# Optimization experiments

Measured on AMD Instinct MI355X. Metric: run time of the kernel, lower is better.

The kernel has to match this reference:

```python
import jax, jax.numpy as jnp
import numpy as np

B, No, Nr, D = 128, 128, 512, 512

def setup_inputs() -> dict:
    key = jax.random.key(0)
    ks = jax.random.split(key, 9)
    s = 1.0 / np.sqrt(2 * D)
    s3 = 1.0 / np.sqrt(3 * D)
    return {
        "obj_vecs": jax.random.normal(ks[0], (B, No, D), jnp.float32),
        "attr_vecs": jax.random.normal(ks[1], (B, No, 2 * D), jnp.float32),
        "rela_vecs": jax.random.normal(ks[2], (B, Nr, D), jnp.float32),
        "edges": jax.random.randint(ks[3], (B, Nr, 2), 0, No, jnp.int64),
        "rela_masks": jnp.ones((B, Nr, 1), jnp.float32),
        "W_att": jax.random.uniform(ks[4], (2 * D, D), jnp.float32, -s, s),
        "b_att": jnp.zeros((D,), jnp.float32),
        "W_attr": jax.random.uniform(ks[5], (2 * D, D), jnp.float32, -s, s),
        "b_attr": jnp.zeros((D,), jnp.float32),
        "W_rela": jax.random.uniform(ks[6], (3 * D, D), jnp.float32, -s3, s3),
        "b_rela": jnp.zeros((D,), jnp.float32),
    }

def reference(obj_vecs, attr_vecs, rela_vecs, edges, rela_masks,
              W_att, b_att, W_attr, b_attr, W_rela, b_rela):
    b, no, d = obj_vecs.shape
    # attr projection: (B,No,2d) -> (B,No,d)
    attr = attr_vecs @ W_att + b_att
    # flatten to 2d with per-batch edge offsets
    obj2 = obj_vecs.reshape(-1, d)
    attr2 = attr.reshape(-1, d)
    rela2 = rela_vecs.reshape(-1, d)
    off = (jnp.arange(b, dtype=edges.dtype) * no)[:, None, None]
    e = (edges + off).reshape(-1, 2)
    # attr branch: cat(obj, attr) -> Linear -> ReLU (+ dropout is identity at eval) + residual
    new_attr = jax.nn.relu(jnp.concatenate([obj2, attr2], -1) @ W_attr + b_attr) + attr2
    # rela branch (rela_gnn_type == 0): cat(s, rela, o)
    s_vecs = obj2[e[:, 0]]
    o_vecs = obj2[e[:, 1]]
    t = jnp.concatenate([s_vecs, rela2, o_vecs], -1)
    new_rela = jax.nn.relu(t @ W_rela + b_rela) + rela2
    new_obj = obj_vecs  # passed through unchanged
    return (new_obj,
            new_attr.reshape(b, no, d),
            new_rela.reshape(b, -1, d) * rela_masks)
```

## Files before the change

### kernel.cpp

```cpp
#include <hip/hip_runtime.h>
#include <hip/hip_bf16.h>
#include <stdint.h>

#define C_B   128
#define C_NO  128
#define C_NR  512
#define C_D   512

typedef __attribute__((ext_vector_type(8))) short  short8;
typedef __attribute__((ext_vector_type(4))) float  floatx4;

__device__ __forceinline__ void load_lds16(const void* g, void* lds) {
  __builtin_amdgcn_global_load_lds(
      (const __attribute__((address_space(1))) void*)g,
      (__attribute__((address_space(3))) void*)lds, 16, 0, 0);
}

__device__ __forceinline__ short bfs(float x) {
  __hip_bfloat16 h = __float2bfloat16(x);
  return *reinterpret_cast<short*>(&h);
}

__global__ void transpose_cvt_k(const float* __restrict__ W,
                                __hip_bfloat16* __restrict__ WT, int K, int N) {
  __shared__ float tile[32][33];
  const int k0 = blockIdx.x * 32;
  const int n0 = blockIdx.y * 32;
  const int tx = threadIdx.x & 31;
  const int ty = threadIdx.x >> 5;
#pragma unroll
  for (int i = ty; i < 32; i += 8)
    tile[i][tx] = W[(size_t)(k0 + i) * N + n0 + tx];
  __syncthreads();
#pragma unroll
  for (int i = ty; i < 32; i += 8)
    WT[(size_t)(n0 + i) * K + k0 + tx] = __float2bfloat16(tile[tx][i]);
}

__global__ void copy16_k(const uint4* __restrict__ src, uint4* __restrict__ dst) {
  const size_t i = (size_t)blockIdx.x * blockDim.x + threadIdx.x;
  dst[i] = src[i];
}

template <int MODE, int K>
__global__ __launch_bounds__(256) void gemm_k(
    const float* __restrict__ A0,
    const float* __restrict__ A1,
    const int* __restrict__ edges,
    const __hip_bfloat16* __restrict__ WT,
    const float* __restrict__ bias,
    const float* __restrict__ resid,
    const float* __restrict__ mask,
    float* __restrict__ Cout) {
  constexpr int BK = 32;
  __shared__ __align__(16) __hip_bfloat16 As[128 * BK];
  __shared__ __align__(16) __hip_bfloat16 Bs[128 * BK];
  __shared__ int sRow[128];
  __shared__ int oRow[128];

  const int t = threadIdx.x;
  const int lane = t & 63;
  const int w = t >> 6;
  const int m0 = blockIdx.y * 128;
  const int n0 = blockIdx.x * 128;

  if constexpr (MODE == 2) {
    if (t < 128) {
      const int r = m0 + t;
      const int b = r >> 9;
      sRow[t] = b * C_NO + edges[2 * r];
      oRow[t] = b * C_NO + edges[2 * r + 1];
    }
    __syncthreads();
  }

  const int aRow = t >> 2;
  const int aCol = (t & 3) * 8;

  floatx4 acc[4][4];
#pragma unroll
  for (int i = 0; i < 4; ++i)
#pragma unroll
    for (int j = 0; j < 4; ++j) acc[i][j] = (floatx4)0.0f;

  const int wm = (w >> 1) * 64;
  const int wn = (w & 1) * 64;
  const int fm = lane & 15;
  const int kq = (lane >> 4) * 8;

  for (int kt = 0; kt < K; kt += BK) {
#pragma unroll
    for (int j = 0; j < 2; ++j)
      load_lds16(WT + (size_t)(n0 + j * 64 + aRow) * K + kt + aCol,
                 &Bs[j * 2048 + w * 512]);
#pragma unroll
    for (int j = 0; j < 2; ++j) {
      const int m = j * 64 + aRow;
      const int kg = kt + aCol;
      const float* srcA;
      if constexpr (MODE == 0) {
        srcA = A0 + (size_t)(m0 + m) * K + kg;
      } else if constexpr (MODE == 1) {
        srcA = (kg < C_D) ? A0 + (size_t)(m0 + m) * C_D + kg
                          : A1 + (size_t)(m0 + m) * C_D + (kg - C_D);
      } else {
        const int region = kg >> 9;
        if (region == 0)
          srcA = A0 + (size_t)sRow[m] * C_D + kg;
        else if (region == 1)
          srcA = A1 + (size_t)(m0 + m) * C_D + (kg - C_D);
        else
          srcA = A0 + (size_t)oRow[m] * C_D + (kg - 2 * C_D);
      }
      const float4 f0 = *reinterpret_cast<const float4*>(srcA);
      const float4 f1 = *reinterpret_cast<const float4*>(srcA + 4);
      short8 v;
      v[0] = bfs(f0.x); v[1] = bfs(f0.y); v[2] = bfs(f0.z); v[3] = bfs(f0.w);
      v[4] = bfs(f1.x); v[5] = bfs(f1.y); v[6] = bfs(f1.z); v[7] = bfs(f1.w);
      *reinterpret_cast<short8*>(&As[j * 2048 + t * 8]) = v;
    }
    __syncthreads();

    short8 af[4], bf[4];
#pragma unroll
    for (int mi = 0; mi < 4; ++mi)
      af[mi] = *reinterpret_cast<const short8*>(&As[(wm + mi * 16 + fm) * BK + kq]);
#pragma unroll
    for (int ni = 0; ni < 4; ++ni)
      bf[ni] = *reinterpret_cast<const short8*>(&Bs[(wn + ni * 16 + fm) * BK + kq]);
#pragma unroll
    for (int mi = 0; mi < 4; ++mi)
#pragma unroll
      for (int ni = 0; ni < 4; ++ni)
        acc[mi][ni] =
            __builtin_amdgcn_mfma_f32_16x16x32_bf16(af[mi], bf[ni], acc[mi][ni], 0, 0, 0);
    __syncthreads();
  }

  float bv[4];
#pragma unroll
  for (int ni = 0; ni < 4; ++ni)
    bv[ni] = bias[n0 + wn + ni * 16 + fm];

#pragma unroll
  for (int mi = 0; mi < 4; ++mi) {
    const int rb = m0 + wm + mi * 16 + (lane >> 4) * 4;
#pragma unroll
    for (int i = 0; i < 4; ++i) {
      const int cm = rb + i;
      float mv = 1.0f;
      if constexpr (MODE == 2) mv = mask[cm];
#pragma unroll
      for (int ni = 0; ni < 4; ++ni) {
        const int cn = n0 + wn + ni * 16 + fm;
        float v = acc[mi][ni][i] + bv[ni];
        if constexpr (MODE == 0) {
          Cout[(size_t)cm * C_D + cn] = v;
        } else {
          v = fmaxf(v, 0.0f) + resid[(size_t)cm * C_D + cn];
          if constexpr (MODE == 2) v *= mv;
          Cout[(size_t)cm * C_D + cn] = v;
        }
      }
    }
  }
}

extern "C" void kernel_launch(void* const* d_in, const int* in_sizes, int n_in,
                              void* d_out, int out_size, void* d_ws, size_t ws_size,
                              hipStream_t stream) {
  const float* obj       = (const float*)d_in[0];
  const float* attr_vecs = (const float*)d_in[1];
  const float* rela      = (const float*)d_in[2];
  const int*   edges     = (const int*)d_in[3];
  const float* masks     = (const float*)d_in[4];
  const float* W_att     = (const float*)d_in[5];
  const float* b_att     = (const float*)d_in[6];
  const float* W_attr    = (const float*)d_in[7];
  const float* b_attr    = (const float*)d_in[8];
  const float* W_rela    = (const float*)d_in[9];
  const float* b_rela    = (const float*)d_in[10];

  float* out      = (float*)d_out;
  float* out_obj  = out;
  float* out_attr = out + 8388608;
  float* out_rela = out + 16777216;

  float*          attrS   = out_rela;
  __hip_bfloat16* WT_att  = (__hip_bfloat16*)(out_rela + 8388608);
  __hip_bfloat16* WT_attr = (__hip_bfloat16*)(out_rela + 8650752);
  __hip_bfloat16* WT_rela = (__hip_bfloat16*)out_obj;

  transpose_cvt_k<<<dim3(32, 16), 256, 0, stream>>>(W_att, WT_att, 1024, 512);
  transpose_cvt_k<<<dim3(32, 16), 256, 0, stream>>>(W_attr, WT_attr, 1024, 512);
  transpose_cvt_k<<<dim3(48, 16), 256, 0, stream>>>(W_rela, WT_rela, 1536, 512);

  gemm_k<0, 1024><<<dim3(4, 128), 256, 0, stream>>>(
      attr_vecs, nullptr, nullptr, WT_att, b_att, nullptr, nullptr, attrS);

  gemm_k<1, 1024><<<dim3(4, 128), 256, 0, stream>>>(
      obj, attrS, nullptr, WT_attr, b_attr, attrS, nullptr, out_attr);

  gemm_k<2, 1536><<<dim3(4, 512), 256, 0, stream>>>(
      obj, rela, edges, WT_rela, b_rela, rela, masks, out_rela);

  copy16_k<<<8192, 256, 0, stream>>>((const uint4*)obj, (uint4*)out_obj);
}
```

Baseline: 698.7 us.

## Pre-convert GEMM activations to bf16 and load A tiles via direct LDS loads

Adds a bulk fp32-to-bf16 conversion kernel for obj and attr_vecs, and has the attention GEMM also write a bf16 copy of its output. The three GEMMs then fetch most A-tile data as bf16 through global_load_lds, instead of loading fp32 and converting per tile in registers. Only the rela segment still converts in-kernel. This halves A-operand bytes for the heavily re-read gathered object rows and cuts per-tile conversion ALU work, at the cost of two extra conversion passes and a restructured scratch layout inside the output buffer. Edge-row indices now live in registers instead of shared memory, which removes one barrier.

```diff
diff --git a/kernel.cpp b/kernel.cpp
--- a/kernel.cpp
+++ b/kernel.cpp
@@ -37,6 +37,17 @@
     WT[(size_t)(n0 + i) * K + k0 + tx] = __float2bfloat16(tile[tx][i]);
 }
 
+__global__ void cvt_bf16_k(const float* __restrict__ src,
+                           __hip_bfloat16* __restrict__ dst) {
+  const size_t i = (size_t)blockIdx.x * blockDim.x + threadIdx.x;
+  const float4 f0 = reinterpret_cast<const float4*>(src)[2 * i];
+  const float4 f1 = reinterpret_cast<const float4*>(src)[2 * i + 1];
+  short8 v;
+  v[0] = bfs(f0.x); v[1] = bfs(f0.y); v[2] = bfs(f0.z); v[3] = bfs(f0.w);
+  v[4] = bfs(f1.x); v[5] = bfs(f1.y); v[6] = bfs(f1.z); v[7] = bfs(f1.w);
+  reinterpret_cast<short8*>(dst)[i] = v;
+}
+
 __global__ void copy16_k(const uint4* __restrict__ src, uint4* __restrict__ dst) {
   const size_t i = (size_t)blockIdx.x * blockDim.x + threadIdx.x;
   dst[i] = src[i];
@@ -44,19 +55,19 @@
 
 template <int MODE, int K>
 __global__ __launch_bounds__(256) void gemm_k(
-    const float* __restrict__ A0,
-    const float* __restrict__ A1,
+    const __hip_bfloat16* __restrict__ A0,
+    const __hip_bfloat16* __restrict__ A1,
+    const float* __restrict__ Af32,
     const int* __restrict__ edges,
     const __hip_bfloat16* __restrict__ WT,
     const float* __restrict__ bias,
     const float* __restrict__ resid,
     const float* __restrict__ mask,
-    float* __restrict__ Cout) {
+    float* __restrict__ Cout,
+    __hip_bfloat16* __restrict__ CoutBf) {
   constexpr int BK = 32;
   __shared__ __align__(16) __hip_bfloat16 As[128 * BK];
   __shared__ __align__(16) __hip_bfloat16 Bs[128 * BK];
-  __shared__ int sRow[128];
-  __shared__ int oRow[128];
 
   const int t = threadIdx.x;
   const int lane = t & 63;
@@ -64,18 +75,18 @@
   const int m0 = blockIdx.y * 128;
   const int n0 = blockIdx.x * 128;
 
-  if constexpr (MODE == 2) {
-    if (t < 128) {
-      const int r = m0 + t;
-      const int b = r >> 9;
-      sRow[t] = b * C_NO + edges[2 * r];
-      oRow[t] = b * C_NO + edges[2 * r + 1];
-    }
-    __syncthreads();
-  }
-
   const int aRow = t >> 2;
   const int aCol = (t & 3) * 8;
+
+  int sr0 = 0, sr1 = 0, or0 = 0, or1 = 0;
+  if constexpr (MODE == 2) {
+    const int r0 = m0 + aRow;
+    const int r1 = r0 + 64;
+    sr0 = (r0 >> 9) * C_NO + edges[2 * r0];
+    or0 = (r0 >> 9) * C_NO + edges[2 * r0 + 1];
+    sr1 = (r1 >> 9) * C_NO + edges[2 * r1];
+    or1 = (r1 >> 9) * C_NO + edges[2 * r1 + 1];
+  }
 
   floatx4 acc[4][4];
 #pragma unroll
@@ -95,29 +106,31 @@
                  &Bs[j * 2048 + w * 512]);
 #pragma unroll
     for (int j = 0; j < 2; ++j) {
-      const int m = j * 64 + aRow;
       const int kg = kt + aCol;
-      const float* srcA;
       if constexpr (MODE == 0) {
-        srcA = A0 + (size_t)(m0 + m) * K + kg;
+        load_lds16(A0 + (size_t)(m0 + j * 64 + aRow) * K + kg,
+                   &As[j * 2048 + w * 512]);
       } else if constexpr (MODE == 1) {
-        srcA = (kg < C_D) ? A0 + (size_t)(m0 + m) * C_D + kg
-                          : A1 + (size_t)(m0 + m) * C_D + (kg - C_D);
+        const __hip_bfloat16* s =
+            (kg < C_D) ? A0 + (size_t)(m0 + j * 64 + aRow) * C_D + kg
+                       : A1 + (size_t)(m0 + j * 64 + aRow) * C_D + (kg - C_D);
+        load_lds16(s, &As[j * 2048 + w * 512]);
       } else {
         const int region = kg >> 9;
-        if (region == 0)
-          srcA = A0 + (size_t)sRow[m] * C_D + kg;
-        else if (region == 1)
-          srcA = A1 + (size_t)(m0 + m) * C_D + (kg - C_D);
-        else
-          srcA = A0 + (size_t)oRow[m] * C_D + (kg - 2 * C_D);
+        if (region == 1) {
+          const float* srcA = Af32 + (size_t)(m0 + j * 64 + aRow) * C_D + (kg - C_D);
+          const float4 f0 = *reinterpret_cast<const float4*>(srcA);
+          const float4 f1 = *reinterpret_cast<const float4*>(srcA + 4);
+          short8 v;
+          v[0] = bfs(f0.x); v[1] = bfs(f0.y); v[2] = bfs(f0.z); v[3] = bfs(f0.w);
+          v[4] = bfs(f1.x); v[5] = bfs(f1.y); v[6] = bfs(f1.z); v[7] = bfs(f1.w);
+          *reinterpret_cast<short8*>(&As[j * 2048 + t * 8]) = v;
+        } else {
+          const int row = (region == 0) ? (j ? sr1 : sr0) : (j ? or1 : or0);
+          const int col = (region == 0) ? kg : (kg - 2 * C_D);
+          load_lds16(A0 + (size_t)row * C_D + col, &As[j * 2048 + w * 512]);
+        }
       }
-      const float4 f0 = *reinterpret_cast<const float4*>(srcA);
-      const float4 f1 = *reinterpret_cast<const float4*>(srcA + 4);
-      short8 v;
-      v[0] = bfs(f0.x); v[1] = bfs(f0.y); v[2] = bfs(f0.z); v[3] = bfs(f0.w);
-      v[4] = bfs(f1.x); v[5] = bfs(f1.y); v[6] = bfs(f1.z); v[7] = bfs(f1.w);
-      *reinterpret_cast<short8*>(&As[j * 2048 + t * 8]) = v;
     }
     __syncthreads();
 
@@ -156,6 +169,7 @@
         float v = acc[mi][ni][i] + bv[ni];
         if constexpr (MODE == 0) {
           Cout[(size_t)cm * C_D + cn] = v;
+          CoutBf[(size_t)cm * C_D + cn] = __float2bfloat16(v);
         } else {
           v = fmaxf(v, 0.0f) + resid[(size_t)cm * C_D + cn];
           if constexpr (MODE == 2) v *= mv;
@@ -186,23 +200,32 @@
   float* out_attr = out + 8388608;
   float* out_rela = out + 16777216;
 
-  float*          attrS   = out_rela;
-  __hip_bfloat16* WT_att  = (__hip_bfloat16*)(out_rela + 8388608);
-  __hip_bfloat16* WT_attr = (__hip_bfloat16*)(out_rela + 8650752);
-  __hip_bfloat16* WT_rela = (__hip_bfloat16*)out_obj;
+  __hip_bfloat16* obj_bf   = (__hip_bfloat16*)out_obj;
+  __hip_bfloat16* WT_rela  = (__hip_bfloat16*)(out_obj + 4194304);
+  __hip_bfloat16* attr_bf  = (__hip_bfloat16*)out_rela;
+  __hip_bfloat16* attrS_bf = (__hip_bfloat16*)(out_rela + 8388608);
+  __hip_bfloat16* WT_attr  = (__hip_bfloat16*)(out_rela + 33030144);
+  __hip_bfloat16* WT_att   = (__hip_bfloat16*)(out_rela + 33292288);
+  float*          attrS    = out_attr;
 
   transpose_cvt_k<<<dim3(32, 16), 256, 0, stream>>>(W_att, WT_att, 1024, 512);
   transpose_cvt_k<<<dim3(32, 16), 256, 0, stream>>>(W_attr, WT_attr, 1024, 512);
   transpose_cvt_k<<<dim3(48, 16), 256, 0, stream>>>(W_rela, WT_rela, 1536, 512);
 
+  cvt_bf16_k<<<4096, 256, 0, stream>>>(obj, obj_bf);
+  cvt_bf16_k<<<8192, 256, 0, stream>>>(attr_vecs, attr_bf);
+
   gemm_k<0, 1024><<<dim3(4, 128), 256, 0, stream>>>(
-      attr_vecs, nullptr, nullptr, WT_att, b_att, nullptr, nullptr, attrS);
+      attr_bf, nullptr, nullptr, nullptr, WT_att, b_att, nullptr, nullptr,
+      attrS, attrS_bf);
 
   gemm_k<1, 1024><<<dim3(4, 128), 256, 0, stream>>>(
-      obj, attrS, nullptr, WT_attr, b_attr, attrS, nullptr, out_attr);
+      obj_bf, attrS_bf, nullptr, nullptr, WT_attr, b_attr, attrS, nullptr,
+      out_attr, nullptr);
 
   gemm_k<2, 1536><<<dim3(4, 512), 256, 0, stream>>>(
-      obj, rela, edges, WT_rela, b_rela, rela, masks, out_rela);
+      obj_bf, nullptr, rela, edges, WT_rela, b_rela, rela, masks,
+      out_rela, nullptr);
 
   copy16_k<<<8192, 256, 0, stream>>>((const uint4*)obj, (uint4*)out_obj);
 }
```

New measurement: 660.2 us. 5.5% less time.
